# Kernel tuning notes

Hardware: AMD Instinct MI355X
Metric: run time of the kernel (lower is better)

## Reference

```python
import jax, jax.numpy as jnp
import numpy as np

N = 100000
NLAYERS = 4
NPROP = 2
NGRAPHS = 50


def gcn_conv(x, edge_index, W, b):
    """PyG GCNConv: h = x@W; out[d] = sum_e norm_e * h[src_e] (+ self loops), norm = D^-1/2 A_hat D^-1/2."""
    n = x.shape[0]
    loop = jnp.arange(n, dtype=edge_index.dtype)
    src = jnp.concatenate([edge_index[0], loop])
    dst = jnp.concatenate([edge_index[1], loop])
    deg = jax.ops.segment_sum(jnp.ones(src.shape[0], x.dtype), dst, num_segments=n)
    dinv = jax.lax.rsqrt(deg)  # deg >= 1 thanks to self loops
    norm = (dinv[src] * dinv[dst])[:, None]
    h = x @ W
    return jax.ops.segment_sum(h[src] * norm, dst, num_segments=n) + b


def setup_inputs() -> dict:
    key = jax.random.key(0)
    ks = jax.random.split(key, 16)
    inp = {
        "x": jax.random.normal(ks[0], (N, 16), jnp.float32),
        "feature_mtx_static": jax.random.normal(ks[1], (N, 32), jnp.float32),
        "edge_index": jax.random.randint(ks[2], (2, 400000), 0, N, jnp.int32),
        "inner_edges": jax.random.randint(ks[3], (NLAYERS, 2, 300000), 0, N, jnp.int32),
        "forward_edges": jax.random.randint(ks[4], (NLAYERS, 2, 300000), 0, N, jnp.int32),
        "backward_edges": jax.random.randint(ks[5], (NLAYERS, 2, 300000), 0, N, jnp.int32),
        "layers": jax.random.randint(ks[6], (N,), 0, NLAYERS, jnp.int32),
        "batch": jnp.sort(jax.random.randint(ks[7], (N,), 0, NGRAPHS, jnp.int32)),
        "W_up": jax.random.normal(ks[8], (16, 256), jnp.float32) * 0.25,
        "b_up": jax.random.normal(ks[9], (256,), jnp.float32) * 0.02,
        "W_in": jax.random.normal(ks[10], (288, 256), jnp.float32) * 0.06,
        "b_in": jax.random.normal(ks[11], (256,), jnp.float32) * 0.02,
        "W_fw": jax.random.normal(ks[12], (288, 256), jnp.float32) * 0.06,
        "b_fw": jax.random.normal(ks[13], (256,), jnp.float32) * 0.02,
        "W_lin": jax.random.normal(ks[14], (256, 1), jnp.float32) * 0.06,
        "b_lin": jax.random.normal(ks[15], (1,), jnp.float32) * 0.02,
    }
    return inp


def reference(x, feature_mtx_static, edge_index, inner_edges, forward_edges,
              backward_edges, layers, batch, W_up, b_up, W_in, b_in,
              W_fw, b_fw, W_lin, b_lin):
    def addstatic(h):
        return jnp.concatenate([h, feature_mtx_static], axis=1)

    x = gcn_conv(x, edge_index, W_up, b_up)
    partial_inner = x  # placeholder; overwritten in forward sweep
    for _ in range(NPROP):
        for il in range(NLAYERS):
            layermask = layers == il
            partial_inner = gcn_conv(addstatic(x), inner_edges[il], W_in, b_in)
            x = jnp.where(layermask[:, None], partial_inner, x)
            next_layer_mask = layers == il + 1
            partial_forward = gcn_conv(addstatic(x), forward_edges[il], W_fw, b_fw)
            x = jnp.where(next_layer_mask[:, None], partial_forward, x)
        x = jax.nn.relu(x)
        for il in range(NLAYERS - 1, -1, -1):
            # NOTE: original code computes forward_conv on backward_edges here but
            # assigns from the stale `partial_inner` (dead compute skipped).
            previous_layer_mask = layers == il - 1
            x = jnp.where(previous_layer_mask[:, None], partial_inner, x)
            layermask = layers == il
            partial_backward = gcn_conv(addstatic(x), inner_edges[il], W_in, b_in)
            x = jnp.where(layermask[:, None], partial_backward, x)
        x = jax.nn.relu(x)

    pooled = jax.ops.segment_sum(x, batch, num_segments=NGRAPHS)  # [G, 256]
    return pooled @ W_lin + b_lin  # [G, 1]
```

## Files before the change

kernel.cpp:

```cpp
#include <hip/hip_runtime.h>

#define N_NODES 100000
#define NLAYERS 4
#define NPROP 2
#define NGRAPHS 50
#define NE_MAIN 400000
#define NE_SET 300000
#define NSETS 9
#define CSR_TOTAL (NE_MAIN + 8 * NE_SET)
#define ASTR 296
#define WFSZ (9 * 16 * 512)
#define PCHUNK 4096
#define NCHK 25

typedef __attribute__((ext_vector_type(8))) short bf8_t;
typedef __attribute__((ext_vector_type(8))) unsigned short us8_t;
typedef __attribute__((ext_vector_type(4))) float f4_t;

__device__ __align__(16) unsigned short g_x[(size_t)N_NODES * 256];
__device__ __align__(16) unsigned short g_pi[(size_t)N_NODES * 256];
__device__ __align__(16) unsigned short g_fsb[(size_t)N_NODES * 32];
__device__ __align__(16) float g_agg16[(size_t)N_NODES * 16];
__device__ __align__(16) float g_dinv[NSETS * N_NODES];
__device__ __align__(16) float g_pooled[NGRAPHS * 256];
__device__ __align__(16) unsigned short g_Wfh[2 * WFSZ];
__device__ __align__(16) unsigned short g_Wfl[2 * WFSZ];
__device__ int g_deg[NSETS * N_NODES];
__device__ int g_degf[NSETS * N_NODES];
__device__ int g_cur[NSETS * N_NODES];
__device__ int g_off[NSETS * (N_NODES + 1)];
__device__ int g_part[NSETS * NCHK];
__device__ int g_csrs[CSR_TOTAL];
__device__ int g_cnt[4];
__device__ int g_lists[NLAYERS * N_NODES];

__host__ __device__ inline int csr_base(int slot) {
    return slot == 0 ? 0 : NE_MAIN + (slot - 1) * NE_SET;
}

__device__ inline unsigned short f2bf(float f) {
    unsigned u = __float_as_uint(f);
    return (unsigned short)((u + 0x7fffu + ((u >> 16) & 1u)) >> 16);
}
__device__ inline float bf2f(unsigned short b) {
    return __uint_as_float(((unsigned)b) << 16);
}

__device__ inline void edge_decode(int t, const int* ei, const int* inner, const int* fwd,
                                   int& slot, const int*& es, const int*& ed, int& e) {
    if (t < NE_MAIN) {
        slot = 0; e = t; es = ei; ed = ei + NE_MAIN;
    } else {
        int r = t - NE_MAIN;
        int grp = r / NE_SET;
        e = r - grp * NE_SET;
        slot = 1 + grp;
        const int* base = (grp < 4) ? (inner + grp * 2 * NE_SET)
                                    : (fwd + (grp - 4) * 2 * NE_SET);
        es = base; ed = base + NE_SET;
    }
}

__device__ inline int csr_keep(int slot, int ld) {
    if (slot == 0 || slot == 4) return 1;
    if (slot <= 3) return ld == slot - 1;
    if (slot <= 7) return ld == slot - 4;
    return 0;
}


__global__ __launch_bounds__(256) void k_init() {
    int i = blockIdx.x * blockDim.x + threadIdx.x;
    if (i < NSETS * N_NODES) { g_deg[i] = 0; g_degf[i] = 0; }
    if (i < NGRAPHS * 256) g_pooled[i] = 0.f;
    if (i < 4) g_cnt[i] = 0;
}

__global__ __launch_bounds__(256) void k_fsb(const float* __restrict__ fs) {
    int i = blockIdx.x * blockDim.x + threadIdx.x;
    if (i < N_NODES * 32) g_fsb[i] = f2bf(fs[i]);
}

__global__ __launch_bounds__(256) void k_count_all(const int* __restrict__ ei,
                                                   const int* __restrict__ inner,
                                                   const int* __restrict__ fwd,
                                                   const int* __restrict__ layers) {
    int t = blockIdx.x * blockDim.x + threadIdx.x;
    if (t >= CSR_TOTAL - NE_SET) return;
    int slot, e; const int *es, *ed;
    edge_decode(t, ei, inner, fwd, slot, es, ed, e);
    int d = ed[e];
    atomicAdd(&g_deg[slot * N_NODES + d], 1);
    if (slot == 0 || slot == 4 || csr_keep(slot, layers[d]))
        atomicAdd(&g_degf[slot * N_NODES + d], 1);
}

__global__ __launch_bounds__(256) void k_dinv() {
    int i = blockIdx.x * blockDim.x + threadIdx.x;
    if (i < NSETS * N_NODES) g_dinv[i] = rsqrtf(1.0f + (float)g_deg[i]);
}

__global__ __launch_bounds__(256) void k_wt(const float* __restrict__ W, int which) {
    int t = blockIdx.x * blockDim.x + threadIdx.x;
    if (t >= 288 * 256) return;
    int k = t >> 8, n = t & 255;
    int kb = k >> 5, kq = k & 31, quad = kq >> 3, ke = kq & 7;
    int nt = n >> 4, m = n & 15, lane = quad * 16 + m;
    int idx = which * WFSZ + (kb * 16 + nt) * 512 + lane * 8 + ke;
    float w = W[t];
    unsigned short h = f2bf(w);
    unsigned short l = f2bf(w - bf2f(h));
    g_Wfh[idx] = h;
    g_Wfl[idx] = l;
}


__global__ __launch_bounds__(256) void k_scan_a() {
    int b = blockIdx.x;
    int set = b / NCHK, ch = b % NCHK;
    const int* deg = g_degf + (size_t)set * N_NODES;
    int base = ch * PCHUNK + threadIdx.x * 16;
    int s = 0;
#pragma unroll
    for (int j = 0; j < 16; j++) {
        int id = base + j;
        if (id < N_NODES) s += deg[id];
    }
    __shared__ int sm[256];
    sm[threadIdx.x] = s;
    __syncthreads();
    for (int o = 128; o > 0; o >>= 1) {
        if (threadIdx.x < o) sm[threadIdx.x] += sm[threadIdx.x + o];
        __syncthreads();
    }
    if (threadIdx.x == 0) g_part[b] = sm[0];
}

__global__ __launch_bounds__(1024) void k_scan_b() {
    int wv = threadIdx.x >> 6, lane = threadIdx.x & 63;
    if (wv >= NSETS) return;
    int v = (lane < NCHK) ? g_part[wv * NCHK + lane] : 0;
    int orig = v;
    for (int o = 1; o < 32; o <<= 1) {
        int u = __shfl_up(v, o);
        if (lane >= o) v += u;
    }
    if (lane < NCHK) g_part[wv * NCHK + lane] = v - orig;
}

__global__ __launch_bounds__(256) void k_scan_c() {
    int b = blockIdx.x;
    int set = b / NCHK, ch = b % NCHK;
    const int* deg = g_degf + (size_t)set * N_NODES;
    int* off = g_off + (size_t)set * (N_NODES + 1);
    int* cur = g_cur + (size_t)set * N_NODES;
    int t = threadIdx.x;
    int base = ch * PCHUNK + t * 16;
    int v[16];
    int s = 0;
#pragma unroll
    for (int j = 0; j < 16; j++) {
        int id = base + j;
        v[j] = (id < N_NODES) ? deg[id] : 0;
        s += v[j];
    }
    __shared__ int sm[256];
    sm[t] = s;
    __syncthreads();
    for (int o = 1; o < 256; o <<= 1) {
        int u = (t >= o) ? sm[t - o] : 0;
        __syncthreads();
        sm[t] += u;
        __syncthreads();
    }
    int run = g_part[b] + sm[t] - s;
#pragma unroll
    for (int j = 0; j < 16; j++) {
        int id = base + j;
        if (id < N_NODES) { off[id] = run; cur[id] = run; }
        run += v[j];
    }
}

__global__ __launch_bounds__(256) void k_fill_all(const int* __restrict__ ei,
                                                  const int* __restrict__ inner,
                                                  const int* __restrict__ fwd,
                                                  const int* __restrict__ layers) {
    int t = blockIdx.x * blockDim.x + threadIdx.x;
    if (t >= CSR_TOTAL - NE_SET) return;
    int slot, e; const int *es, *ed;
    edge_decode(t, ei, inner, fwd, slot, es, ed, e);
    int d = ed[e];
    if (!(slot == 0 || slot == 4 || csr_keep(slot, layers[d]))) return;
    int s = es[e];
    int pos = atomicAdd(&g_cur[slot * N_NODES + d], 1);
    g_csrs[csr_base(slot) + pos] = s;
}

__global__ __launch_bounds__(256) void k_lists(const int* __restrict__ layers) {
    __shared__ int lcnt[4];
    __shared__ int lbase[4];
    int i = blockIdx.x * blockDim.x + threadIdx.x;
    if (threadIdx.x < 4) lcnt[threadIdx.x] = 0;
    __syncthreads();
    int l = -1, p = 0;
    if (i < N_NODES) {
        l = layers[i];
        p = atomicAdd(&lcnt[l], 1);
    }
    __syncthreads();
    if (threadIdx.x < 4) lbase[threadIdx.x] = atomicAdd(&g_cnt[threadIdx.x], lcnt[threadIdx.x]);
    __syncthreads();
    if (l >= 0) g_lists[l * N_NODES + lbase[l] + p] = i;
}


__global__ __launch_bounds__(256) void k_gather16(const float* __restrict__ xin) {
    int g = blockIdx.x * blockDim.x + threadIdx.x;
    int i = g >> 4, lane = g & 15;
    if (i >= N_NODES) return;
    float dv = g_dinv[i];
    float acc = dv * dv * xin[i * 16 + lane];
    int e0 = g_off[i], e1 = g_off[i] + g_degf[i];
    for (int e = e0; e < e1; e++) {
        int s = g_csrs[e];
        acc += g_dinv[s] * dv * xin[s * 16 + lane];
    }
    g_agg16[i * 16 + lane] = acc;
}

__global__ __launch_bounds__(256) void k_gemm0(const float* __restrict__ W,
                                               const float* __restrict__ bias) {
    __shared__ float a[128];
    int base = blockIdx.x * 8;
    int t = threadIdx.x;
    if (t < 128) a[t] = g_agg16[base * 16 + t];
    __syncthreads();
    float bb = bias[t];
    for (int r = 0; r < 8; r++) {
        float acc = bb;
#pragma unroll
        for (int k = 0; k < 16; k++) acc += a[r * 16 + k] * W[k * 256 + t];
        g_x[(size_t)(base + r) * 256 + t] = f2bf(acc);
    }
}


__global__ __launch_bounds__(256, 4) void k_conv(int slot, int which,
                                                 const float* __restrict__ bias,
                                                 int layer, int topi) {
    int count = (layer >= 0) ? g_cnt[layer] : N_NODES;
    int base = blockIdx.x * 32;
    if (base >= count) return;
    const unsigned short* Wfh = g_Wfh + (size_t)which * WFSZ;
    const unsigned short* Wfl = g_Wfl + (size_t)which * WFSZ;
    unsigned short* out = topi ? g_pi : g_x;

    __shared__ unsigned short lds_h[32 * ASTR];
    __shared__ unsigned short lds_l[32 * ASTR];
    __shared__ int rows_s[32];
    int t = threadIdx.x;
    if (t < 32) {
        int r = base + t;
        rows_s[t] = (r < count) ? ((layer >= 0) ? g_lists[layer * N_NODES + r] : r) : -1;
    }
    __syncthreads();

    int wv = t >> 6, lane = t & 63;
    int grp = lane >> 4, gl = lane & 15;

    const float* dinv_s = g_dinv + (size_t)slot * N_NODES;
    const int* offp = g_off + (size_t)slot * (N_NODES + 1);
    const int* degfp = g_degf + (size_t)slot * N_NODES;
    int cb = csr_base(slot);
    for (int rr = 0; rr < 2; rr++) {
        int lr = wv * 8 + grp * 2 + rr;
        int row = rows_s[lr];
        float acc0[8], acc1[8], accf[8];
#pragma unroll
        for (int j = 0; j < 8; j++) { acc0[j] = 0.f; acc1[j] = 0.f; accf[j] = 0.f; }
        if (row >= 0) {
            float dvr = dinv_s[row];
            float d2 = dvr * dvr;
            us8_t u0 = *(const us8_t*)&g_x[(size_t)row * 256 + gl * 8];
            us8_t u1 = *(const us8_t*)&g_x[(size_t)row * 256 + 128 + gl * 8];
#pragma unroll
            for (int j = 0; j < 8; j++) { acc0[j] = d2 * bf2f(u0[j]); acc1[j] = d2 * bf2f(u1[j]); }
            if (gl < 4) {
                us8_t uf = *(const us8_t*)&g_fsb[(size_t)row * 32 + gl * 8];
#pragma unroll
                for (int j = 0; j < 8; j++) accf[j] = d2 * bf2f(uf[j]);
            }
            int e0 = offp[row] + cb, e1e = e0 + degfp[row];
            int e = e0;
            for (; e + 1 < e1e; e += 2) {
                int sa = g_csrs[e], sb = g_csrs[e + 1];
                float na = dinv_s[sa] * dvr;
                float nb = dinv_s[sb] * dvr;
                us8_t va0 = *(const us8_t*)&g_x[(size_t)sa * 256 + gl * 8];
                us8_t va1 = *(const us8_t*)&g_x[(size_t)sa * 256 + 128 + gl * 8];
                us8_t vb0 = *(const us8_t*)&g_x[(size_t)sb * 256 + gl * 8];
                us8_t vb1 = *(const us8_t*)&g_x[(size_t)sb * 256 + 128 + gl * 8];
#pragma unroll
                for (int j = 0; j < 8; j++) {
                    acc0[j] += na * bf2f(va0[j]); acc1[j] += na * bf2f(va1[j]);
                    acc0[j] += nb * bf2f(vb0[j]); acc1[j] += nb * bf2f(vb1[j]);
                }
                if (gl < 4) {
                    us8_t fa = *(const us8_t*)&g_fsb[(size_t)sa * 32 + gl * 8];
                    us8_t fb = *(const us8_t*)&g_fsb[(size_t)sb * 32 + gl * 8];
#pragma unroll
                    for (int j = 0; j < 8; j++)
                        accf[j] += na * bf2f(fa[j]) + nb * bf2f(fb[j]);
                }
            }
            if (e < e1e) {
                int sa = g_csrs[e];
                float na = dinv_s[sa] * dvr;
                us8_t va0 = *(const us8_t*)&g_x[(size_t)sa * 256 + gl * 8];
                us8_t va1 = *(const us8_t*)&g_x[(size_t)sa * 256 + 128 + gl * 8];
#pragma unroll
                for (int j = 0; j < 8; j++) {
                    acc0[j] += na * bf2f(va0[j]); acc1[j] += na * bf2f(va1[j]);
                }
                if (gl < 4) {
                    us8_t fa = *(const us8_t*)&g_fsb[(size_t)sa * 32 + gl * 8];
#pragma unroll
                    for (int j = 0; j < 8; j++) accf[j] += na * bf2f(fa[j]);
                }
            }
        }
        us8_t h0, l0, h1, l1;
#pragma unroll
        for (int j = 0; j < 8; j++) {
            h0[j] = f2bf(acc0[j]); l0[j] = f2bf(acc0[j] - bf2f(h0[j]));
            h1[j] = f2bf(acc1[j]); l1[j] = f2bf(acc1[j] - bf2f(h1[j]));
        }
        *(us8_t*)&lds_h[lr * ASTR + gl * 8] = h0;
        *(us8_t*)&lds_h[lr * ASTR + 128 + gl * 8] = h1;
        *(us8_t*)&lds_l[lr * ASTR + gl * 8] = l0;
        *(us8_t*)&lds_l[lr * ASTR + 128 + gl * 8] = l1;
        if (gl < 4) {
            us8_t hf, lf;
#pragma unroll
            for (int j = 0; j < 8; j++) {
                hf[j] = f2bf(accf[j]); lf[j] = f2bf(accf[j] - bf2f(hf[j]));
            }
            *(us8_t*)&lds_h[lr * ASTR + 256 + gl * 8] = hf;
            *(us8_t*)&lds_l[lr * ASTR + 256 + gl * 8] = lf;
        }
    }
    __syncthreads();

    int m = lane & 15, quad = lane >> 4;
    int n0 = wv * 64;
    f4_t acc2[2][4];
#pragma unroll
    for (int rt = 0; rt < 2; rt++)
#pragma unroll
        for (int ct = 0; ct < 4; ct++) acc2[rt][ct] = (f4_t){0.f, 0.f, 0.f, 0.f};

    for (int kb = 0; kb < 9; kb++) {
        int k0 = kb * 32;
        bf8_t ah0 = *(const bf8_t*)&lds_h[m * ASTR + k0 + quad * 8];
        bf8_t al0 = *(const bf8_t*)&lds_l[m * ASTR + k0 + quad * 8];
        bf8_t ah1 = *(const bf8_t*)&lds_h[(16 + m) * ASTR + k0 + quad * 8];
        bf8_t al1 = *(const bf8_t*)&lds_l[(16 + m) * ASTR + k0 + quad * 8];
#pragma unroll
        for (int ct = 0; ct < 4; ct++) {
            int nt = wv * 4 + ct;
            const bf8_t bh = *(const bf8_t*)&Wfh[(kb * 16 + nt) * 512 + lane * 8];
            const bf8_t bl = *(const bf8_t*)&Wfl[(kb * 16 + nt) * 512 + lane * 8];
            acc2[0][ct] = __builtin_amdgcn_mfma_f32_16x16x32_bf16(ah0, bh, acc2[0][ct], 0, 0, 0);
            acc2[0][ct] = __builtin_amdgcn_mfma_f32_16x16x32_bf16(al0, bh, acc2[0][ct], 0, 0, 0);
            acc2[0][ct] = __builtin_amdgcn_mfma_f32_16x16x32_bf16(ah0, bl, acc2[0][ct], 0, 0, 0);
            acc2[1][ct] = __builtin_amdgcn_mfma_f32_16x16x32_bf16(ah1, bh, acc2[1][ct], 0, 0, 0);
            acc2[1][ct] = __builtin_amdgcn_mfma_f32_16x16x32_bf16(al1, bh, acc2[1][ct], 0, 0, 0);
            acc2[1][ct] = __builtin_amdgcn_mfma_f32_16x16x32_bf16(ah1, bl, acc2[1][ct], 0, 0, 0);
        }
    }
#pragma unroll
    for (int rt = 0; rt < 2; rt++) {
#pragma unroll
        for (int r = 0; r < 4; r++) {
            int row = rows_s[rt * 16 + quad * 4 + r];
            if (row < 0) continue;
#pragma unroll
            for (int ct = 0; ct < 4; ct++) {
                int n = n0 + ct * 16 + m;
                out[(size_t)row * 256 + n] = f2bf(acc2[rt][ct][r] + bias[n]);
            }
        }
    }
}


__global__ __launch_bounds__(256) void k_copy_rows(int layer) {
    int w = (blockIdx.x * blockDim.x + threadIdx.x) >> 5;
    int lane = threadIdx.x & 31;
    if (w >= g_cnt[layer]) return;
    int i = g_lists[layer * N_NODES + w];
    *(uint4*)(g_x + (size_t)i * 256 + lane * 8) =
        *(const uint4*)(g_pi + (size_t)i * 256 + lane * 8);
}

__global__ __launch_bounds__(256) void k_relu() {
    int i = blockIdx.x * blockDim.x + threadIdx.x;
    if (i >= N_NODES * 32) return;
    ushort4 a = ((ushort4*)g_x)[i * 2];
    ushort4 b = ((ushort4*)g_x)[i * 2 + 1];
    a.x = (a.x & 0x8000) ? 0 : a.x; a.y = (a.y & 0x8000) ? 0 : a.y;
    a.z = (a.z & 0x8000) ? 0 : a.z; a.w = (a.w & 0x8000) ? 0 : a.w;
    b.x = (b.x & 0x8000) ? 0 : b.x; b.y = (b.y & 0x8000) ? 0 : b.y;
    b.z = (b.z & 0x8000) ? 0 : b.z; b.w = (b.w & 0x8000) ? 0 : b.w;
    ((ushort4*)g_x)[i * 2] = a;
    ((ushort4*)g_x)[i * 2 + 1] = b;
}

__global__ __launch_bounds__(256) void k_pool(const int* __restrict__ batch) {
    __shared__ int bs[128];
    int i0 = blockIdx.x * 128;
    if (threadIdx.x < 128) {
        int i = i0 + threadIdx.x;
        bs[threadIdx.x] = (i < N_NODES) ? batch[i] : -1;
    }
    __syncthreads();
    int c = threadIdx.x;
    int lim = min(128, N_NODES - i0);
    float acc = 0.f;
    int cur = bs[0];
    for (int ii = 0; ii < lim; ii++) {
        int g = bs[ii];
        if (g != cur) { atomicAdd(&g_pooled[cur * 256 + c], acc); acc = 0.f; cur = g; }
        acc += fmaxf(bf2f(g_x[(size_t)(i0 + ii) * 256 + c]), 0.f);
    }
    atomicAdd(&g_pooled[cur * 256 + c], acc);
}

__global__ void k_final(const float* __restrict__ W_lin, const float* __restrict__ b_lin,
                        float* __restrict__ out) {
    int g = blockIdx.x;
    int lane = threadIdx.x;
    float4 p = *(const float4*)(g_pooled + g * 256 + lane * 4);
    float4 w = *(const float4*)(W_lin + lane * 4);
    float s = p.x * w.x + p.y * w.y + p.z * w.z + p.w * w.w;
    for (int o = 32; o > 0; o >>= 1) s += __shfl_down(s, o);
    if (lane == 0) out[g] = s + b_lin[0];
}


extern "C" void kernel_launch(void* const* d_in, const int* in_sizes, int n_in,
                              void* d_out, int out_size, void* d_ws, size_t ws_size,
                              hipStream_t stream) {
    const float* xin   = (const float*)d_in[0];
    const float* fs    = (const float*)d_in[1];
    const int* ei      = (const int*)d_in[2];
    const int* inner   = (const int*)d_in[3];
    const int* fwd     = (const int*)d_in[4];
    const int* layers  = (const int*)d_in[6];
    const int* batch   = (const int*)d_in[7];
    const float* W_up  = (const float*)d_in[8];
    const float* b_up  = (const float*)d_in[9];
    const float* W_in  = (const float*)d_in[10];
    const float* b_in  = (const float*)d_in[11];
    const float* W_fw  = (const float*)d_in[12];
    const float* b_fw  = (const float*)d_in[13];
    const float* W_lin = (const float*)d_in[14];
    const float* b_lin = (const float*)d_in[15];
    float* out = (float*)d_out;

    k_init<<<(NSETS * N_NODES + 255) / 256, 256, 0, stream>>>();
    k_fsb<<<(N_NODES * 32 + 255) / 256, 256, 0, stream>>>(fs);
    k_wt<<<(288 * 256 + 255) / 256, 256, 0, stream>>>(W_in, 0);
    k_wt<<<(288 * 256 + 255) / 256, 256, 0, stream>>>(W_fw, 1);
    k_count_all<<<(CSR_TOTAL - NE_SET + 255) / 256, 256, 0, stream>>>(ei, inner, fwd, layers);
    k_dinv<<<(NSETS * N_NODES + 255) / 256, 256, 0, stream>>>();
    k_scan_a<<<NSETS * NCHK, 256, 0, stream>>>();
    k_scan_b<<<1, 1024, 0, stream>>>();
    k_scan_c<<<NSETS * NCHK, 256, 0, stream>>>();
    k_fill_all<<<(CSR_TOTAL - NE_SET + 255) / 256, 256, 0, stream>>>(ei, inner, fwd, layers);
    k_lists<<<(N_NODES + 255) / 256, 256, 0, stream>>>(layers);

    k_gather16<<<(N_NODES * 16 + 255) / 256, 256, 0, stream>>>(xin);
    k_gemm0<<<N_NODES / 8, 256, 0, stream>>>(W_up, b_up);

    auto conv = [&](int slot, int which, const float* bias, int layer, int topi) {
        k_conv<<<(N_NODES + 31) / 32, 256, 0, stream>>>(slot, which, bias, layer, topi);
    };

    for (int p = 0; p < NPROP; p++) {
        for (int il = 0; il < NLAYERS; il++) {
            if (il < NLAYERS - 1) {
                conv(1 + il, 0, b_in, il, 0);
                conv(5 + il, 1, b_fw, il + 1, 0);
            } else {
                conv(1 + il, 0, b_in, -1, 1);
                k_copy_rows<<<12500, 256, 0, stream>>>(3);
            }
        }
        k_relu<<<(N_NODES * 32 + 255) / 256, 256, 0, stream>>>();
        for (int il = NLAYERS - 1; il >= 0; il--) {
            if (il >= 1) k_copy_rows<<<12500, 256, 0, stream>>>(il - 1);
            conv(1 + il, 0, b_in, il, 0);
        }
        if (p < NPROP - 1)
            k_relu<<<(N_NODES * 32 + 255) / 256, 256, 0, stream>>>();
    }

    k_pool<<<(N_NODES + 127) / 128, 256, 0, stream>>>(batch);
    k_final<<<NGRAPHS, 64, 0, stream>>>(W_lin, b_lin, out);
}
```

Baseline: 1.366 ms.

## Halve conv row tile for occupancy and drop filtered-degree array

The conv kernel now processes 16 rows per block instead of 32, with one aggregation row per thread group. Launch bounds move from 4 to 8 waves and the MFMA loop is cut to a single row tile. The goal is more resident blocks and more parallelism during the latency-bound neighbour gather, at the cost of re-reading each weight fragment for half as many rows. Separately, the filtered degree array and its second atomic are removed: the layer filter is applied during the offset scan, and the conv and gather kernels reuse the raw degree array, which matches the filtered count for the rows they actually visit.

```diff
diff --git a/kernel.cpp b/kernel.cpp
--- a/kernel.cpp
+++ b/kernel.cpp
@@ -26,7 +26,6 @@
 __device__ __align__(16) unsigned short g_Wfh[2 * WFSZ];
 __device__ __align__(16) unsigned short g_Wfl[2 * WFSZ];
 __device__ int g_deg[NSETS * N_NODES];
-__device__ int g_degf[NSETS * N_NODES];
 __device__ int g_cur[NSETS * N_NODES];
 __device__ int g_off[NSETS * (N_NODES + 1)];
 __device__ int g_part[NSETS * NCHK];
@@ -71,7 +70,7 @@
 
 __global__ __launch_bounds__(256) void k_init() {
     int i = blockIdx.x * blockDim.x + threadIdx.x;
-    if (i < NSETS * N_NODES) { g_deg[i] = 0; g_degf[i] = 0; }
+    if (i < NSETS * N_NODES) g_deg[i] = 0;
     if (i < NGRAPHS * 256) g_pooled[i] = 0.f;
     if (i < 4) g_cnt[i] = 0;
 }
@@ -83,16 +82,12 @@
 
 __global__ __launch_bounds__(256) void k_count_all(const int* __restrict__ ei,
                                                    const int* __restrict__ inner,
-                                                   const int* __restrict__ fwd,
-                                                   const int* __restrict__ layers) {
+                                                   const int* __restrict__ fwd) {
     int t = blockIdx.x * blockDim.x + threadIdx.x;
     if (t >= CSR_TOTAL - NE_SET) return;
     int slot, e; const int *es, *ed;
     edge_decode(t, ei, inner, fwd, slot, es, ed, e);
-    int d = ed[e];
-    atomicAdd(&g_deg[slot * N_NODES + d], 1);
-    if (slot == 0 || slot == 4 || csr_keep(slot, layers[d]))
-        atomicAdd(&g_degf[slot * N_NODES + d], 1);
+    atomicAdd(&g_deg[slot * N_NODES + ed[e]], 1);
 }
 
 __global__ __launch_bounds__(256) void k_dinv() {
@@ -115,16 +110,16 @@
 }
 
 
-__global__ __launch_bounds__(256) void k_scan_a() {
+__global__ __launch_bounds__(256) void k_scan_a(const int* __restrict__ layers) {
     int b = blockIdx.x;
     int set = b / NCHK, ch = b % NCHK;
-    const int* deg = g_degf + (size_t)set * N_NODES;
+    const int* deg = g_deg + (size_t)set * N_NODES;
     int base = ch * PCHUNK + threadIdx.x * 16;
     int s = 0;
 #pragma unroll
     for (int j = 0; j < 16; j++) {
         int id = base + j;
-        if (id < N_NODES) s += deg[id];
+        if (id < N_NODES && csr_keep(set, layers[id])) s += deg[id];
     }
     __shared__ int sm[256];
     sm[threadIdx.x] = s;
@@ -148,10 +143,10 @@
     if (lane < NCHK) g_part[wv * NCHK + lane] = v - orig;
 }
 
-__global__ __launch_bounds__(256) void k_scan_c() {
+__global__ __launch_bounds__(256) void k_scan_c(const int* __restrict__ layers) {
     int b = blockIdx.x;
     int set = b / NCHK, ch = b % NCHK;
-    const int* deg = g_degf + (size_t)set * N_NODES;
+    const int* deg = g_deg + (size_t)set * N_NODES;
     int* off = g_off + (size_t)set * (N_NODES + 1);
     int* cur = g_cur + (size_t)set * N_NODES;
     int t = threadIdx.x;
@@ -161,7 +156,7 @@
 #pragma unroll
     for (int j = 0; j < 16; j++) {
         int id = base + j;
-        v[j] = (id < N_NODES) ? deg[id] : 0;
+        v[j] = (id < N_NODES && csr_keep(set, layers[id])) ? deg[id] : 0;
         s += v[j];
     }
     __shared__ int sm[256];
@@ -191,7 +186,7 @@
     int slot, e; const int *es, *ed;
     edge_decode(t, ei, inner, fwd, slot, es, ed, e);
     int d = ed[e];
-    if (!(slot == 0 || slot == 4 || csr_keep(slot, layers[d]))) return;
+    if (!csr_keep(slot, layers[d])) return;
     int s = es[e];
     int pos = atomicAdd(&g_cur[slot * N_NODES + d], 1);
     g_csrs[csr_base(slot) + pos] = s;
@@ -221,7 +216,7 @@
     if (i >= N_NODES) return;
     float dv = g_dinv[i];
     float acc = dv * dv * xin[i * 16 + lane];
-    int e0 = g_off[i], e1 = g_off[i] + g_degf[i];
+    int e0 = g_off[i], e1 = g_off[i] + g_deg[i];
     for (int e = e0; e < e1; e++) {
         int s = g_csrs[e];
         acc += g_dinv[s] * dv * xin[s * 16 + lane];
@@ -246,21 +241,21 @@
 }
 
 
-__global__ __launch_bounds__(256, 4) void k_conv(int slot, int which,
+__global__ __launch_bounds__(256, 8) void k_conv(int slot, int which,
                                                  const float* __restrict__ bias,
                                                  int layer, int topi) {
     int count = (layer >= 0) ? g_cnt[layer] : N_NODES;
-    int base = blockIdx.x * 32;
+    int base = blockIdx.x * 16;
     if (base >= count) return;
     const unsigned short* Wfh = g_Wfh + (size_t)which * WFSZ;
     const unsigned short* Wfl = g_Wfl + (size_t)which * WFSZ;
     unsigned short* out = topi ? g_pi : g_x;
 
-    __shared__ unsigned short lds_h[32 * ASTR];
-    __shared__ unsigned short lds_l[32 * ASTR];
-    __shared__ int rows_s[32];
+    __shared__ unsigned short lds_h[16 * ASTR];
+    __shared__ unsigned short lds_l[16 * ASTR];
+    __shared__ int rows_s[16];
     int t = threadIdx.x;
-    if (t < 32) {
+    if (t < 16) {
         int r = base + t;
         rows_s[t] = (r < count) ? ((layer >= 0) ? g_lists[layer * N_NODES + r] : r) : -1;
     }
@@ -271,10 +266,10 @@
 
     const float* dinv_s = g_dinv + (size_t)slot * N_NODES;
     const int* offp = g_off + (size_t)slot * (N_NODES + 1);
-    const int* degfp = g_degf + (size_t)slot * N_NODES;
+    const int* degp = g_deg + (size_t)slot * N_NODES;
     int cb = csr_base(slot);
-    for (int rr = 0; rr < 2; rr++) {
-        int lr = wv * 8 + grp * 2 + rr;
+    {
+        int lr = wv * 4 + grp;
         int row = rows_s[lr];
         float acc0[8], acc1[8], accf[8];
 #pragma unroll
@@ -291,7 +286,7 @@
 #pragma unroll
                 for (int j = 0; j < 8; j++) accf[j] = d2 * bf2f(uf[j]);
             }
-            int e0 = offp[row] + cb, e1e = e0 + degfp[row];
+            int e0 = offp[row] + cb, e1e = e0 + degp[row];
             int e = e0;
             for (; e + 1 < e1e; e += 2) {
                 int sa = g_csrs[e], sb = g_csrs[e + 1];
@@ -354,42 +349,32 @@
 
     int m = lane & 15, quad = lane >> 4;
     int n0 = wv * 64;
-    f4_t acc2[2][4];
-#pragma unroll
-    for (int rt = 0; rt < 2; rt++)
-#pragma unroll
-        for (int ct = 0; ct < 4; ct++) acc2[rt][ct] = (f4_t){0.f, 0.f, 0.f, 0.f};
+    f4_t acc2[4];
+#pragma unroll
+    for (int ct = 0; ct < 4; ct++) acc2[ct] = (f4_t){0.f, 0.f, 0.f, 0.f};
 
     for (int kb = 0; kb < 9; kb++) {
         int k0 = kb * 32;
-        bf8_t ah0 = *(const bf8_t*)&lds_h[m * ASTR + k0 + quad * 8];
-        bf8_t al0 = *(const bf8_t*)&lds_l[m * ASTR + k0 + quad * 8];
-        bf8_t ah1 = *(const bf8_t*)&lds_h[(16 + m) * ASTR + k0 + quad * 8];
-        bf8_t al1 = *(const bf8_t*)&lds_l[(16 + m) * ASTR + k0 + quad * 8];
+        bf8_t ah = *(const bf8_t*)&lds_h[m * ASTR + k0 + quad * 8];
+        bf8_t al = *(const bf8_t*)&lds_l[m * ASTR + k0 + quad * 8];
 #pragma unroll
         for (int ct = 0; ct < 4; ct++) {
             int nt = wv * 4 + ct;
             const bf8_t bh = *(const bf8_t*)&Wfh[(kb * 16 + nt) * 512 + lane * 8];
             const bf8_t bl = *(const bf8_t*)&Wfl[(kb * 16 + nt) * 512 + lane * 8];
-            acc2[0][ct] = __builtin_amdgcn_mfma_f32_16x16x32_bf16(ah0, bh, acc2[0][ct], 0, 0, 0);
-            acc2[0][ct] = __builtin_amdgcn_mfma_f32_16x16x32_bf16(al0, bh, acc2[0][ct], 0, 0, 0);
-            acc2[0][ct] = __builtin_amdgcn_mfma_f32_16x16x32_bf16(ah0, bl, acc2[0][ct], 0, 0, 0);
-            acc2[1][ct] = __builtin_amdgcn_mfma_f32_16x16x32_bf16(ah1, bh, acc2[1][ct], 0, 0, 0);
-            acc2[1][ct] = __builtin_amdgcn_mfma_f32_16x16x32_bf16(al1, bh, acc2[1][ct], 0, 0, 0);
-            acc2[1][ct] = __builtin_amdgcn_mfma_f32_16x16x32_bf16(ah1, bl, acc2[1][ct], 0, 0, 0);
-        }
-    }
-#pragma unroll
-    for (int rt = 0; rt < 2; rt++) {
-#pragma unroll
-        for (int r = 0; r < 4; r++) {
-            int row = rows_s[rt * 16 + quad * 4 + r];
-            if (row < 0) continue;
-#pragma unroll
-            for (int ct = 0; ct < 4; ct++) {
-                int n = n0 + ct * 16 + m;
-                out[(size_t)row * 256 + n] = f2bf(acc2[rt][ct][r] + bias[n]);
-            }
+            acc2[ct] = __builtin_amdgcn_mfma_f32_16x16x32_bf16(ah, bh, acc2[ct], 0, 0, 0);
+            acc2[ct] = __builtin_amdgcn_mfma_f32_16x16x32_bf16(al, bh, acc2[ct], 0, 0, 0);
+            acc2[ct] = __builtin_amdgcn_mfma_f32_16x16x32_bf16(ah, bl, acc2[ct], 0, 0, 0);
+        }
+    }
+#pragma unroll
+    for (int r = 0; r < 4; r++) {
+        int row = rows_s[quad * 4 + r];
+        if (row < 0) continue;
+#pragma unroll
+        for (int ct = 0; ct < 4; ct++) {
+            int n = n0 + ct * 16 + m;
+            out[(size_t)row * 256 + n] = f2bf(acc2[ct][r] + bias[n]);
         }
     }
 }
@@ -473,11 +458,11 @@
     k_fsb<<<(N_NODES * 32 + 255) / 256, 256, 0, stream>>>(fs);
     k_wt<<<(288 * 256 + 255) / 256, 256, 0, stream>>>(W_in, 0);
     k_wt<<<(288 * 256 + 255) / 256, 256, 0, stream>>>(W_fw, 1);
-    k_count_all<<<(CSR_TOTAL - NE_SET + 255) / 256, 256, 0, stream>>>(ei, inner, fwd, layers);
+    k_count_all<<<(CSR_TOTAL - NE_SET + 255) / 256, 256, 0, stream>>>(ei, inner, fwd);
     k_dinv<<<(NSETS * N_NODES + 255) / 256, 256, 0, stream>>>();
-    k_scan_a<<<NSETS * NCHK, 256, 0, stream>>>();
+    k_scan_a<<<NSETS * NCHK, 256, 0, stream>>>(layers);
     k_scan_b<<<1, 1024, 0, stream>>>();
-    k_scan_c<<<NSETS * NCHK, 256, 0, stream>>>();
+    k_scan_c<<<NSETS * NCHK, 256, 0, stream>>>(layers);
     k_fill_all<<<(CSR_TOTAL - NE_SET + 255) / 256, 256, 0, stream>>>(ei, inner, fwd, layers);
     k_lists<<<(N_NODES + 255) / 256, 256, 0, stream>>>(layers);
 
@@ -485,7 +470,7 @@
     k_gemm0<<<N_NODES / 8, 256, 0, stream>>>(W_up, b_up);
 
     auto conv = [&](int slot, int which, const float* bias, int layer, int topi) {
-        k_conv<<<(N_NODES + 31) / 32, 256, 0, stream>>>(slot, which, bias, layer, topi);
+        k_conv<<<(N_NODES + 15) / 16, 256, 0, stream>>>(slot, which, bias, layer, topi);
     };
 
     for (int p = 0; p < NPROP; p++) {
```

Measured after the change: 1.570 ms. +15.0%, slower.
